# Optimization experiments

Measured on AMD Instinct MI355X. Metric: run time of the kernel, lower is better.

## Reference

```python
import jax, jax.numpy as jnp
import numpy as np

D_LOB = 128
D_HAWKES = 32
N_HEADS = 4
HEAD_DIM = D_LOB // N_HEADS
LN_EPS = 1e-5


def setup_inputs() -> dict:
    key = jax.random.key(0)
    ks = jax.random.split(key, 10)
    B, T = 8, 2048
    s = lambda fan_in: 1.0 / np.sqrt(fan_in)
    return {
        "lob": jax.random.normal(ks[0], (B, T, D_LOB), dtype=jnp.float32),
        "hawkes": jax.random.normal(ks[1], (B, T, D_HAWKES), dtype=jnp.float32),
        # hawkes_proj: Linear(d_hawkes, d_lob)
        "Wp": jax.random.uniform(ks[2], (D_LOB, D_HAWKES), jnp.float32, -s(D_HAWKES), s(D_HAWKES)),
        "bp": jnp.zeros((D_LOB,), jnp.float32),
        # MultiheadAttention packed in-projection (3*d_lob, d_lob) and out-projection
        "Win": jax.random.uniform(ks[3], (3 * D_LOB, D_LOB), jnp.float32, -s(D_LOB), s(D_LOB)),
        "bin_": jnp.zeros((3 * D_LOB,), jnp.float32),
        "Wo": jax.random.uniform(ks[4], (D_LOB, D_LOB), jnp.float32, -s(D_LOB), s(D_LOB)),
        "bo": jnp.zeros((D_LOB,), jnp.float32),
        # LayerNorm affine params
        "gamma": jnp.ones((D_LOB,), jnp.float32),
        "beta": jnp.zeros((D_LOB,), jnp.float32),
    }


def reference(lob, hawkes, Wp, bp, Win, bin_, Wo, bo, gamma, beta):
    B, T, _ = lob.shape
    # hawkes_proj
    h = hawkes @ Wp.T + bp  # (B, T, d_lob)
    # packed QKV projection (query=lob, key=value=h)
    q = lob @ Win[:D_LOB].T + bin_[:D_LOB]
    k = h @ Win[D_LOB:2 * D_LOB].T + bin_[D_LOB:2 * D_LOB]
    v = h @ Win[2 * D_LOB:].T + bin_[2 * D_LOB:]
    # split heads -> (B, H, T, hd)
    split = lambda x: x.reshape(B, T, N_HEADS, HEAD_DIM).transpose(0, 2, 1, 3)
    q, k, v = split(q), split(k), split(v)
    scale = 1.0 / np.sqrt(HEAD_DIM).astype(np.float32)
    scores = jnp.einsum("bhqd,bhkd->bhqk", q * scale, k)  # (B, H, T, T)
    attn = jax.nn.softmax(scores, axis=-1)
    # dropout(p=0.1) omitted: reference is eval/inference mode
    ctx = jnp.einsum("bhqk,bhkd->bhqd", attn, v)  # (B, H, T, hd)
    ctx = ctx.transpose(0, 2, 1, 3).reshape(B, T, D_LOB)
    fused = ctx @ Wo.T + bo
    # residual + LayerNorm
    x = lob + fused
    mu = jnp.mean(x, axis=-1, keepdims=True)
    var = jnp.mean(jnp.square(x - mu), axis=-1, keepdims=True)
    out = (x - mu) * jax.lax.rsqrt(var + LN_EPS) * gamma + beta
    attn_w = jnp.mean(attn, axis=1)  # average over heads (B, T, T)
    return out, attn_w
```

## Files before the change

kernel.cpp:

```cpp
#include <hip/hip_runtime.h>
#include <hip/hip_bf16.h>

#define TT 2048
#define BB 8
#define DD 128
#define HH 4
#define BT (BB*TT)
#define BH (BB*HH)
#define SCALE 0.1767766952966369f
#define S2LOG (SCALE * 1.4426950408889634f)

typedef __attribute__((ext_vector_type(8))) short short8;
typedef __attribute__((ext_vector_type(4))) short short4v;
typedef __attribute__((ext_vector_type(4))) float f32x4;
typedef __hip_bfloat16 bf16;

#define MFMA16(a,b,c) __builtin_amdgcn_mfma_f32_16x16x32_bf16(a,b,c,0,0,0)

static __device__ inline short8 ldg8(const bf16* p) {
  return *reinterpret_cast<const short8*>(p);
}
static __device__ inline short4v ldg4(const bf16* p) {
  return *reinterpret_cast<const short4v*>(p);
}
static __device__ inline float b2f(bf16 x) { return __bfloat162float(x); }
static __device__ inline short f2bs(float x) {
  bf16 h = __float2bfloat16(x);
  return *reinterpret_cast<short*>(&h);
}
static __device__ inline short8 ldcvt8(const float* p) {
  f32x4 f0 = *reinterpret_cast<const f32x4*>(p);
  f32x4 f1 = *reinterpret_cast<const f32x4*>(p + 4);
  short8 r;
  #pragma unroll
  for (int i = 0; i < 4; ++i) { r[i] = f2bs(f0[i]); r[4+i] = f2bs(f1[i]); }
  return r;
}
static __device__ inline short8 pack_v(const bf16* vp) {
  short4v lo = ldg4(vp);
  short4v hi = ldg4(vp + 16);
  short8 r;
  #pragma unroll
  for (int j = 0; j < 4; ++j) { r[j] = lo[j]; r[4+j] = hi[j]; }
  return r;
}

__global__ __launch_bounds__(256) void proj_kernel(
    const float* __restrict__ lob, const float* __restrict__ hawkes,
    const float* __restrict__ Wp, const float* __restrict__ bp,
    const float* __restrict__ Win, const float* __restrict__ binp,
    bf16* __restrict__ qg, bf16* __restrict__ kg, bf16* __restrict__ vtg) {
  __shared__ bf16 hT[32*136];
  __shared__ bf16 vT[128*40];
  int tid = threadIdx.x;
  int wave = tid >> 6, lane = tid & 63;
  int lr = lane & 15, lq = lane >> 4;
  int r0 = blockIdx.x * 32;
  int b  = r0 >> 11, t0 = r0 & 2047;
  f32x4 z = {0.f,0.f,0.f,0.f};

  short8 alob[2][4], ahk[2];
  #pragma unroll
  for (int mt = 0; mt < 2; ++mt) {
    const float* lp = lob + (size_t)(r0 + mt*16 + lr)*128;
    #pragma unroll
    for (int kt = 0; kt < 4; ++kt) alob[mt][kt] = ldcvt8(lp + kt*32 + lq*8);
    ahk[mt] = ldcvt8(hawkes + (size_t)(r0 + mt*16 + lr)*32 + lq*8);
  }

  for (int nt = wave; nt < 8; nt += 4) {
    int cn = nt*16;
    short8 bfrag = ldcvt8(Wp + (size_t)(cn + lr)*32 + lq*8);
    float bias = bp[cn + lr];
    #pragma unroll
    for (int mt = 0; mt < 2; ++mt) {
      f32x4 c = MFMA16(ahk[mt], bfrag, z);
      #pragma unroll
      for (int r = 0; r < 4; ++r)
        hT[(mt*16 + lq*4 + r)*136 + cn + lr] = __float2bfloat16(c[r] + bias);
    }
  }
  __syncthreads();

  short8 ah[2][4];
  #pragma unroll
  for (int mt = 0; mt < 2; ++mt)
    #pragma unroll
    for (int kt = 0; kt < 4; ++kt)
      ah[mt][kt] = *reinterpret_cast<const short8*>(&hT[(mt*16 + lr)*136 + kt*32 + lq*8]);

  for (int nt = wave; nt < 24; nt += 4) {
    int which = nt >> 3;
    int c = (nt & 7)*16 + lr;
    const float* wrow = Win + (size_t)(which*128 + c)*128;
    float bias = binp[which*128 + c];
    f32x4 acc0 = z, acc1 = z;
    #pragma unroll
    for (int kt = 0; kt < 4; ++kt) {
      short8 bfrag = ldcvt8(wrow + kt*32 + lq*8);
      if (which == 0) {
        acc0 = MFMA16(alob[0][kt], bfrag, acc0);
        acc1 = MFMA16(alob[1][kt], bfrag, acc1);
      } else {
        acc0 = MFMA16(ah[0][kt], bfrag, acc0);
        acc1 = MFMA16(ah[1][kt], bfrag, acc1);
      }
    }
    int head = c >> 5, dd = c & 31;
    #pragma unroll
    for (int mt = 0; mt < 2; ++mt) {
      f32x4 acc = mt ? acc1 : acc0;
      #pragma unroll
      for (int r = 0; r < 4; ++r) {
        int row = mt*16 + lq*4 + r;
        float val = acc[r] + bias;
        if (which == 0)
          qg[((size_t)(b*HH + head)*TT + t0 + row)*32 + dd] = __float2bfloat16(val);
        else if (which == 1)
          kg[((size_t)(b*HH + head)*TT + t0 + row)*32 + dd] = __float2bfloat16(val);
        else
          vT[c*40 + row] = __float2bfloat16(val);
      }
    }
  }
  __syncthreads();

  {
    int dd = tid >> 1, half = tid & 1;
    int bh = b*HH + (dd >> 5);
    short8 s0 = *reinterpret_cast<const short8*>(&vT[dd*40 + half*16]);
    short8 s1 = *reinterpret_cast<const short8*>(&vT[dd*40 + half*16 + 8]);
    bf16* dst = vtg + ((size_t)bh*32 + (dd & 31))*TT + t0 + half*16;
    *reinterpret_cast<short8*>(dst) = s0;
    *reinterpret_cast<short8*>(dst + 8) = s1;
  }
}

__global__ __launch_bounds__(256) void attn_kernel(const bf16* __restrict__ qg,
    const bf16* __restrict__ kg, const bf16* __restrict__ vtg,
    float* __restrict__ attn_out, float* __restrict__ ctxg) {
  int wg = (blockIdx.x & 7)*64 + (blockIdx.x >> 3);
  int b = wg >> 6, qt = wg & 63;
  int head = threadIdx.x >> 6, lane = threadIdx.x & 63;
  int lr = lane & 15, lq = lane >> 4;
  int bh = b*HH + head;
  __shared__ float plds[2][4][32*68];
  const bf16* qp = qg + ((size_t)(bh*TT) + qt*32)*32;
  const bf16* kb = kg + (size_t)(bh*TT)*32;
  const bf16* vb = vtg + (size_t)(bh*32)*TT;
  short8 a0 = ldg8(qp + lr*32 + lq*8);
  short8 a1 = ldg8(qp + (16+lr)*32 + lq*8);
  f32x4 z = {0.f,0.f,0.f,0.f};

  float rs0 = 0.f, rs1 = 0.f;
  for (int kt = 0; kt < 64; ++kt) {
    const bf16* kp = kb + (size_t)(kt*32)*32;
    short8 bk0 = ldg8(kp + lr*32 + lq*8);
    short8 bk1 = ldg8(kp + (16+lr)*32 + lq*8);
    f32x4 s0a = MFMA16(bk0, a0, z);
    f32x4 s0b = MFMA16(bk0, a1, z);
    f32x4 s1a = MFMA16(bk1, a0, z);
    f32x4 s1b = MFMA16(bk1, a1, z);
    #pragma unroll
    for (int r = 0; r < 4; ++r) {
      rs0 += exp2f(s0a[r]*S2LOG) + exp2f(s1a[r]*S2LOG);
      rs1 += exp2f(s0b[r]*S2LOG) + exp2f(s1b[r]*S2LOG);
    }
  }
  rs0 += __shfl_xor(rs0, 16, 64); rs0 += __shfl_xor(rs0, 32, 64);
  rs1 += __shfl_xor(rs1, 16, 64); rs1 += __shfl_xor(rs1, 32, 64);
  float lb0 = -log2f(rs0);
  float lb1 = -log2f(rs1);

  f32x4 acc00 = z, acc01 = z, acc10 = z, acc11 = z;
  short8 kf[2][4];
  short8 vf[2][4];
  #pragma unroll
  for (int s = 0; s < 4; ++s)
    kf[0][s] = ldg8(kb + (size_t)(s*16 + lr)*32 + lq*8);
  #pragma unroll
  for (int t32 = 0; t32 < 2; ++t32)
    #pragma unroll
    for (int dt = 0; dt < 2; ++dt)
      vf[0][t32*2+dt] = pack_v(vb + (size_t)(dt*16 + lr)*TT + t32*32 + lq*4);

  int rr = (int)threadIdx.x >> 3, c0 = ((int)threadIdx.x & 7)*8;
  float* awdst = attn_out + ((size_t)(b*TT + qt*32 + rr))*TT + c0;

  for (int kt0 = 0; kt0 < 32; kt0 += 2) {
    #pragma unroll
    for (int par = 0; par < 2; ++par) {
      int kt2 = kt0 + par;
      int kbase = kt2*64;
      if (kt2 < 31) {
        int nb = kbase + 64;
        #pragma unroll
        for (int s = 0; s < 4; ++s)
          kf[par^1][s] = ldg8(kb + (size_t)(nb + s*16 + lr)*32 + lq*8);
        #pragma unroll
        for (int t32 = 0; t32 < 2; ++t32)
          #pragma unroll
          for (int dt = 0; dt < 2; ++dt)
            vf[par^1][t32*2+dt] = pack_v(vb + (size_t)(dt*16 + lr)*TT + nb + t32*32 + lq*4);
      }
      short8 ap[2][2];
      #pragma unroll
      for (int qtile = 0; qtile < 2; ++qtile) {
        float lb = qtile ? lb1 : lb0;
        const short8& aq = qtile ? a1 : a0;
        #pragma unroll
        for (int s = 0; s < 4; ++s) {
          f32x4 sv = MFMA16(kf[par][s], aq, z);
          f32x4 p4;
          #pragma unroll
          for (int r = 0; r < 4; ++r) p4[r] = exp2f(fmaf(sv[r], S2LOG, lb));
          *reinterpret_cast<f32x4*>(
              &plds[par][head][(qtile*16 + lr)*68 + s*16 + lq*4]) = p4;
          #pragma unroll
          for (int r = 0; r < 4; ++r)
            ap[qtile][s>>1][(s&1)*4 + r] = f2bs(p4[r]);
        }
      }
      __syncthreads();
      {
        const float* p0 = &plds[par][0][rr*68 + c0];
        f32x4 u0 = *reinterpret_cast<const f32x4*>(p0);
        f32x4 u1 = *reinterpret_cast<const f32x4*>(p0 + 4);
        #pragma unroll
        for (int h = 1; h < 4; ++h) {
          const float* ph = &plds[par][h][rr*68 + c0];
          u0 += *reinterpret_cast<const f32x4*>(ph);
          u1 += *reinterpret_cast<const f32x4*>(ph + 4);
        }
        float* dst = awdst + kbase;
        *reinterpret_cast<f32x4*>(dst)     = u0 * 0.25f;
        *reinterpret_cast<f32x4*>(dst + 4) = u1 * 0.25f;
      }
      #pragma unroll
      for (int t32 = 0; t32 < 2; ++t32) {
        acc00 = MFMA16(ap[0][t32], vf[par][t32*2+0], acc00);
        acc01 = MFMA16(ap[0][t32], vf[par][t32*2+1], acc01);
        acc10 = MFMA16(ap[1][t32], vf[par][t32*2+0], acc10);
        acc11 = MFMA16(ap[1][t32], vf[par][t32*2+1], acc11);
      }
    }
  }
  #pragma unroll
  for (int r = 0; r < 4; ++r) {
    int row0 = lq*4 + r, row1 = row0 + 16;
    size_t base0 = ((size_t)(b*TT + qt*32 + row0))*128 + head*32;
    size_t base1 = ((size_t)(b*TT + qt*32 + row1))*128 + head*32;
    ctxg[base0 + lr]      = acc00[r];
    ctxg[base0 + 16 + lr] = acc01[r];
    ctxg[base1 + lr]      = acc10[r];
    ctxg[base1 + 16 + lr] = acc11[r];
  }
}

__global__ __launch_bounds__(256) void outln_kernel(const float* __restrict__ ctxg,
    const float* __restrict__ lob, const float* __restrict__ Wo,
    const float* __restrict__ bo, const float* __restrict__ gamma,
    const float* __restrict__ beta, float* __restrict__ outg) {
  __shared__ float sWo[128*132];
  __shared__ float sP[384];
  __shared__ float sCtx[4][128];
  __shared__ float sLob[4][128];
  int tid = threadIdx.x;
  for (int i = tid; i < 128*32; i += 256) {
    int c = i >> 5, d4 = (i & 31)*4;
    *reinterpret_cast<f32x4*>(&sWo[c*132 + d4]) =
        *reinterpret_cast<const f32x4*>(&Wo[(size_t)c*128 + d4]);
  }
  if (tid < 128) {
    sP[tid] = bo[tid]; sP[128+tid] = gamma[tid]; sP[256+tid] = beta[tid];
  }
  __syncthreads();
  int wave = tid >> 6, lane = tid & 63;
  for (int it = 0; it < 8; ++it) {
    int row = blockIdx.x*32 + it*4 + wave;
    const float* cg = ctxg + (size_t)row*128;
    const float* lg = lob + (size_t)row*128;
    sCtx[wave][lane]    = cg[lane];
    sCtx[wave][64+lane] = cg[64+lane];
    sLob[wave][lane]    = lg[lane];
    sLob[wave][64+lane] = lg[64+lane];
    float x0 = sP[lane] + sLob[wave][lane];
    float x1 = sP[64+lane] + sLob[wave][64+lane];
    const float* w0 = &sWo[lane*132];
    const float* w1 = &sWo[(64+lane)*132];
    const float* cx = sCtx[wave];
    #pragma unroll 8
    for (int d4 = 0; d4 < 32; ++d4) {
      f32x4 cv  = *reinterpret_cast<const f32x4*>(cx + d4*4);
      f32x4 wv0 = *reinterpret_cast<const f32x4*>(w0 + d4*4);
      f32x4 wv1 = *reinterpret_cast<const f32x4*>(w1 + d4*4);
      x0 += cv[0]*wv0[0] + cv[1]*wv0[1] + cv[2]*wv0[2] + cv[3]*wv0[3];
      x1 += cv[0]*wv1[0] + cv[1]*wv1[1] + cv[2]*wv1[2] + cv[3]*wv1[3];
    }
    float sum = x0 + x1;
    #pragma unroll
    for (int m = 1; m < 64; m <<= 1) sum += __shfl_xor(sum, m, 64);
    float mu = sum * (1.0f/128.0f);
    float d0 = x0 - mu, d1 = x1 - mu;
    float vs = d0*d0 + d1*d1;
    #pragma unroll
    for (int m = 1; m < 64; m <<= 1) vs += __shfl_xor(vs, m, 64);
    float rstd = rsqrtf(vs*(1.0f/128.0f) + 1e-5f);
    outg[(size_t)row*128 + lane]      = d0*rstd*sP[128+lane] + sP[256+lane];
    outg[(size_t)row*128 + 64 + lane] = d1*rstd*sP[192+lane] + sP[320+lane];
  }
}

extern "C" void kernel_launch(void* const* d_in, const int* in_sizes, int n_in,
                              void* d_out, int out_size, void* d_ws, size_t ws_size,
                              hipStream_t stream) {
  const float* lob    = (const float*)d_in[0];
  const float* hawkes = (const float*)d_in[1];
  const float* Wp     = (const float*)d_in[2];
  const float* bp     = (const float*)d_in[3];
  const float* Win    = (const float*)d_in[4];
  const float* binp   = (const float*)d_in[5];
  const float* Wo     = (const float*)d_in[6];
  const float* bo     = (const float*)d_in[7];
  const float* gamma  = (const float*)d_in[8];
  const float* beta   = (const float*)d_in[9];
  float* outg = (float*)d_out;
  float* attn_out = outg + (size_t)BT*128;

  char* ws = (char*)d_ws;
  bf16*  qg   = (bf16*)(ws);
  bf16*  kg   = (bf16*)(ws + (size_t)4*1024*1024);
  bf16*  vtg  = (bf16*)(ws + (size_t)8*1024*1024);
  float* ctxg = (float*)(ws + (size_t)12*1024*1024);

  proj_kernel<<<BT/32, 256, 0, stream>>>(lob, hawkes, Wp, bp, Win, binp, qg, kg, vtg);
  attn_kernel<<<BB*(TT/32), 256, 0, stream>>>(qg, kg, vtg, attn_out, ctxg);
  outln_kernel<<<512, 256, 0, stream>>>(ctxg, lob, Wo, bo, gamma, beta, outg);
}
```

Baseline: 322.8 us.

## Split attention keys across waves, average heads in registers, MFMA out-projection

The attention kernel now has each wave handle all four heads over a disjoint strided subset of key tiles. This lets the head-averaged attention weights be summed in registers and written straight to global memory, removing the per-tile LDS exchange and __syncthreads. Row sums and partial context accumulators are reduced across waves through shared memory, and the context is stored as bf16. The output-projection kernel switches to bf16 MFMA with a shared-memory LayerNorm and a single-pass variance, at the cost of extra rounding error and higher register pressure from 32 accumulators per wave.

```diff
diff --git a/kernel.cpp b/kernel.cpp
--- a/kernel.cpp
+++ b/kernel.cpp
@@ -1,5 +1,6 @@
 #include <hip/hip_runtime.h>
 #include <hip/hip_bf16.h>
+#include <math.h>
 
 #define TT 2048
 #define BB 8
@@ -23,7 +24,6 @@
 static __device__ inline short4v ldg4(const bf16* p) {
   return *reinterpret_cast<const short4v*>(p);
 }
-static __device__ inline float b2f(bf16 x) { return __bfloat162float(x); }
 static __device__ inline short f2bs(float x) {
   bf16 h = __float2bfloat16(x);
   return *reinterpret_cast<short*>(&h);
@@ -34,14 +34,6 @@
   short8 r;
   #pragma unroll
   for (int i = 0; i < 4; ++i) { r[i] = f2bs(f0[i]); r[4+i] = f2bs(f1[i]); }
-  return r;
-}
-static __device__ inline short8 pack_v(const bf16* vp) {
-  short4v lo = ldg4(vp);
-  short4v hi = ldg4(vp + 16);
-  short8 r;
-  #pragma unroll
-  for (int j = 0; j < 4; ++j) { r[j] = lo[j]; r[4+j] = hi[j]; }
   return r;
 }
 
@@ -138,176 +130,213 @@
 
 __global__ __launch_bounds__(256) void attn_kernel(const bf16* __restrict__ qg,
     const bf16* __restrict__ kg, const bf16* __restrict__ vtg,
-    float* __restrict__ attn_out, float* __restrict__ ctxg) {
-  int wg = (blockIdx.x & 7)*64 + (blockIdx.x >> 3);
-  int b = wg >> 6, qt = wg & 63;
-  int head = threadIdx.x >> 6, lane = threadIdx.x & 63;
+    float* __restrict__ attn_out, bf16* __restrict__ ctxg) {
+  int wgid = (blockIdx.x & 7)*64 + (blockIdx.x >> 3);
+  int b = wgid >> 6, qt = wgid & 63;
+  int wave = threadIdx.x >> 6, lane = threadIdx.x & 63;
   int lr = lane & 15, lq = lane >> 4;
-  int bh = b*HH + head;
-  __shared__ float plds[2][4][32*68];
-  const bf16* qp = qg + ((size_t)(bh*TT) + qt*32)*32;
-  const bf16* kb = kg + (size_t)(bh*TT)*32;
-  const bf16* vb = vtg + (size_t)(bh*32)*TT;
-  short8 a0 = ldg8(qp + lr*32 + lq*8);
-  short8 a1 = ldg8(qp + (16+lr)*32 + lq*8);
+  __shared__ float sRed[4][16*132];
+  float* sdl = &sRed[0][0];
+  const bf16* qb = qg + ((size_t)(b*HH)*TT + (size_t)qt*32)*32;
+  const bf16* kb = kg + (size_t)(b*HH)*TT*32;
+  const bf16* vb = vtg + (size_t)(b*HH)*32*TT;
   f32x4 z = {0.f,0.f,0.f,0.f};
 
-  float rs0 = 0.f, rs1 = 0.f;
-  for (int kt = 0; kt < 64; ++kt) {
-    const bf16* kp = kb + (size_t)(kt*32)*32;
-    short8 bk0 = ldg8(kp + lr*32 + lq*8);
-    short8 bk1 = ldg8(kp + (16+lr)*32 + lq*8);
-    f32x4 s0a = MFMA16(bk0, a0, z);
-    f32x4 s0b = MFMA16(bk0, a1, z);
-    f32x4 s1a = MFMA16(bk1, a0, z);
-    f32x4 s1b = MFMA16(bk1, a1, z);
-    #pragma unroll
-    for (int r = 0; r < 4; ++r) {
-      rs0 += exp2f(s0a[r]*S2LOG) + exp2f(s1a[r]*S2LOG);
-      rs1 += exp2f(s0b[r]*S2LOG) + exp2f(s1b[r]*S2LOG);
-    }
-  }
-  rs0 += __shfl_xor(rs0, 16, 64); rs0 += __shfl_xor(rs0, 32, 64);
-  rs1 += __shfl_xor(rs1, 16, 64); rs1 += __shfl_xor(rs1, 32, 64);
-  float lb0 = -log2f(rs0);
-  float lb1 = -log2f(rs1);
-
-  f32x4 acc00 = z, acc01 = z, acc10 = z, acc11 = z;
-  short8 kf[2][4];
-  short8 vf[2][4];
-  #pragma unroll
-  for (int s = 0; s < 4; ++s)
-    kf[0][s] = ldg8(kb + (size_t)(s*16 + lr)*32 + lq*8);
-  #pragma unroll
-  for (int t32 = 0; t32 < 2; ++t32)
-    #pragma unroll
-    for (int dt = 0; dt < 2; ++dt)
-      vf[0][t32*2+dt] = pack_v(vb + (size_t)(dt*16 + lr)*TT + t32*32 + lq*4);
-
-  int rr = (int)threadIdx.x >> 3, c0 = ((int)threadIdx.x & 7)*8;
-  float* awdst = attn_out + ((size_t)(b*TT + qt*32 + rr))*TT + c0;
-
-  for (int kt0 = 0; kt0 < 32; kt0 += 2) {
-    #pragma unroll
-    for (int par = 0; par < 2; ++par) {
-      int kt2 = kt0 + par;
-      int kbase = kt2*64;
-      if (kt2 < 31) {
-        int nb = kbase + 64;
-        #pragma unroll
-        for (int s = 0; s < 4; ++s)
-          kf[par^1][s] = ldg8(kb + (size_t)(nb + s*16 + lr)*32 + lq*8);
-        #pragma unroll
-        for (int t32 = 0; t32 < 2; ++t32)
-          #pragma unroll
-          for (int dt = 0; dt < 2; ++dt)
-            vf[par^1][t32*2+dt] = pack_v(vb + (size_t)(dt*16 + lr)*TT + nb + t32*32 + lq*4);
-      }
-      short8 ap[2][2];
-      #pragma unroll
-      for (int qtile = 0; qtile < 2; ++qtile) {
-        float lb = qtile ? lb1 : lb0;
-        const short8& aq = qtile ? a1 : a0;
-        #pragma unroll
-        for (int s = 0; s < 4; ++s) {
-          f32x4 sv = MFMA16(kf[par][s], aq, z);
-          f32x4 p4;
-          #pragma unroll
-          for (int r = 0; r < 4; ++r) p4[r] = exp2f(fmaf(sv[r], S2LOG, lb));
-          *reinterpret_cast<f32x4*>(
-              &plds[par][head][(qtile*16 + lr)*68 + s*16 + lq*4]) = p4;
-          #pragma unroll
-          for (int r = 0; r < 4; ++r)
-            ap[qtile][s>>1][(s&1)*4 + r] = f2bs(p4[r]);
+  short8 aq[4][2];
+  #pragma unroll
+  for (int h = 0; h < 4; ++h)
+    #pragma unroll
+    for (int m = 0; m < 2; ++m)
+      aq[h][m] = ldg8(qb + (size_t)h*TT*32 + (m*16 + lr)*32 + lq*8);
+
+  float rs[4][2] = {{0.f,0.f},{0.f,0.f},{0.f,0.f},{0.f,0.f}};
+  for (int i = 0; i < 32; ++i) {
+    int s = wave + i*4;
+    #pragma unroll
+    for (int h = 0; h < 4; ++h) {
+      short8 kf = ldg8(kb + (size_t)h*TT*32 + (s*16 + lr)*32 + lq*8);
+      #pragma unroll
+      for (int m = 0; m < 2; ++m) {
+        f32x4 sv = MFMA16(kf, aq[h][m], z);
+        #pragma unroll
+        for (int r = 0; r < 4; ++r) rs[h][m] += exp2f(sv[r]*S2LOG);
+      }
+    }
+  }
+  #pragma unroll
+  for (int h = 0; h < 4; ++h)
+    #pragma unroll
+    for (int m = 0; m < 2; ++m) {
+      rs[h][m] += __shfl_xor(rs[h][m], 16, 64);
+      rs[h][m] += __shfl_xor(rs[h][m], 32, 64);
+    }
+  if (lq == 0) {
+    #pragma unroll
+    for (int h = 0; h < 4; ++h)
+      #pragma unroll
+      for (int m = 0; m < 2; ++m)
+        sdl[wave*128 + h*32 + m*16 + lr] = rs[h][m];
+  }
+  __syncthreads();
+  float lb[4][2];
+  #pragma unroll
+  for (int h = 0; h < 4; ++h)
+    #pragma unroll
+    for (int m = 0; m < 2; ++m) {
+      float t = sdl[0*128 + h*32 + m*16 + lr] + sdl[1*128 + h*32 + m*16 + lr]
+              + sdl[2*128 + h*32 + m*16 + lr] + sdl[3*128 + h*32 + m*16 + lr];
+      lb[h][m] = -log2f(t);
+    }
+  __syncthreads();
+
+  f32x4 acc[4][2][2];
+  #pragma unroll
+  for (int h = 0; h < 4; ++h)
+    #pragma unroll
+    for (int m = 0; m < 2; ++m)
+      #pragma unroll
+      for (int dt = 0; dt < 2; ++dt) acc[h][m][dt] = z;
+
+  float* awr = attn_out + (size_t)(b*TT + qt*32)*TT;
+  for (int i = 0; i < 16; ++i) {
+    int sA = wave + i*8, sB = sA + 4;
+    f32x4 awA0 = z, awA1 = z, awB0 = z, awB1 = z;
+    #pragma unroll
+    for (int h = 0; h < 4; ++h) {
+      const bf16* kph = kb + (size_t)h*TT*32;
+      short8 kfA = ldg8(kph + (sA*16 + lr)*32 + lq*8);
+      short8 kfB = ldg8(kph + (sB*16 + lr)*32 + lq*8);
+      short8 apm[2];
+      #pragma unroll
+      for (int m = 0; m < 2; ++m) {
+        f32x4 svA = MFMA16(kfA, aq[h][m], z);
+        f32x4 svB = MFMA16(kfB, aq[h][m], z);
+        f32x4 pA, pB;
+        #pragma unroll
+        for (int r = 0; r < 4; ++r) {
+          pA[r] = exp2f(fmaf(svA[r], S2LOG, lb[h][m]));
+          pB[r] = exp2f(fmaf(svB[r], S2LOG, lb[h][m]));
         }
-      }
-      __syncthreads();
-      {
-        const float* p0 = &plds[par][0][rr*68 + c0];
-        f32x4 u0 = *reinterpret_cast<const f32x4*>(p0);
-        f32x4 u1 = *reinterpret_cast<const f32x4*>(p0 + 4);
-        #pragma unroll
-        for (int h = 1; h < 4; ++h) {
-          const float* ph = &plds[par][h][rr*68 + c0];
-          u0 += *reinterpret_cast<const f32x4*>(ph);
-          u1 += *reinterpret_cast<const f32x4*>(ph + 4);
-        }
-        float* dst = awdst + kbase;
-        *reinterpret_cast<f32x4*>(dst)     = u0 * 0.25f;
-        *reinterpret_cast<f32x4*>(dst + 4) = u1 * 0.25f;
-      }
-      #pragma unroll
-      for (int t32 = 0; t32 < 2; ++t32) {
-        acc00 = MFMA16(ap[0][t32], vf[par][t32*2+0], acc00);
-        acc01 = MFMA16(ap[0][t32], vf[par][t32*2+1], acc01);
-        acc10 = MFMA16(ap[1][t32], vf[par][t32*2+0], acc10);
-        acc11 = MFMA16(ap[1][t32], vf[par][t32*2+1], acc11);
-      }
-    }
-  }
-  #pragma unroll
-  for (int r = 0; r < 4; ++r) {
-    int row0 = lq*4 + r, row1 = row0 + 16;
-    size_t base0 = ((size_t)(b*TT + qt*32 + row0))*128 + head*32;
-    size_t base1 = ((size_t)(b*TT + qt*32 + row1))*128 + head*32;
-    ctxg[base0 + lr]      = acc00[r];
-    ctxg[base0 + 16 + lr] = acc01[r];
-    ctxg[base1 + lr]      = acc10[r];
-    ctxg[base1 + 16 + lr] = acc11[r];
-  }
-}
-
-__global__ __launch_bounds__(256) void outln_kernel(const float* __restrict__ ctxg,
+        if (m == 0) { awA0 += pA; awB0 += pB; } else { awA1 += pA; awB1 += pB; }
+        short8 ap;
+        #pragma unroll
+        for (int r = 0; r < 4; ++r) { ap[r] = f2bs(pA[r]); ap[4+r] = f2bs(pB[r]); }
+        apm[m] = ap;
+      }
+      const bf16* vph = vb + (size_t)h*32*TT;
+      #pragma unroll
+      for (int dt = 0; dt < 2; ++dt) {
+        const bf16* vp = vph + (size_t)(dt*16 + lr)*TT;
+        short4v lo = ldg4(vp + sA*16 + lq*4);
+        short4v hi = ldg4(vp + sB*16 + lq*4);
+        short8 vf;
+        #pragma unroll
+        for (int j = 0; j < 4; ++j) { vf[j] = lo[j]; vf[4+j] = hi[j]; }
+        acc[h][0][dt] = MFMA16(apm[0], vf, acc[h][0][dt]);
+        acc[h][1][dt] = MFMA16(apm[1], vf, acc[h][1][dt]);
+      }
+    }
+    *reinterpret_cast<f32x4*>(awr + (size_t)lr*TT      + sA*16 + lq*4) = awA0 * 0.25f;
+    *reinterpret_cast<f32x4*>(awr + (size_t)lr*TT      + sB*16 + lq*4) = awB0 * 0.25f;
+    *reinterpret_cast<f32x4*>(awr + (size_t)(16+lr)*TT + sA*16 + lq*4) = awA1 * 0.25f;
+    *reinterpret_cast<f32x4*>(awr + (size_t)(16+lr)*TT + sB*16 + lq*4) = awB1 * 0.25f;
+  }
+
+  bf16* cbase = ctxg + (size_t)(b*TT + qt*32)*128;
+  #pragma unroll
+  for (int m = 0; m < 2; ++m) {
+    #pragma unroll
+    for (int h = 0; h < 4; ++h)
+      #pragma unroll
+      for (int dt = 0; dt < 2; ++dt)
+        #pragma unroll
+        for (int r = 0; r < 4; ++r)
+          sRed[wave][(lq*4 + r)*132 + h*32 + dt*16 + lr] = acc[h][m][dt][r];
+    __syncthreads();
+    {
+      int t = threadIdx.x;
+      int q = t >> 4, d0 = (t & 15)*8;
+      float v[8];
+      #pragma unroll
+      for (int j = 0; j < 8; ++j)
+        v[j] = sRed[0][q*132 + d0 + j] + sRed[1][q*132 + d0 + j]
+             + sRed[2][q*132 + d0 + j] + sRed[3][q*132 + d0 + j];
+      short8 o;
+      #pragma unroll
+      for (int j = 0; j < 8; ++j) o[j] = f2bs(v[j]);
+      *reinterpret_cast<short8*>(cbase + (size_t)(m*16 + q)*128 + d0) = o;
+    }
+    __syncthreads();
+  }
+}
+
+__global__ __launch_bounds__(256) void outln_kernel(const bf16* __restrict__ ctxg,
     const float* __restrict__ lob, const float* __restrict__ Wo,
     const float* __restrict__ bo, const float* __restrict__ gamma,
     const float* __restrict__ beta, float* __restrict__ outg) {
-  __shared__ float sWo[128*132];
-  __shared__ float sP[384];
-  __shared__ float sCtx[4][128];
-  __shared__ float sLob[4][128];
-  int tid = threadIdx.x;
-  for (int i = tid; i < 128*32; i += 256) {
-    int c = i >> 5, d4 = (i & 31)*4;
-    *reinterpret_cast<f32x4*>(&sWo[c*132 + d4]) =
-        *reinterpret_cast<const f32x4*>(&Wo[(size_t)c*128 + d4]);
-  }
-  if (tid < 128) {
-    sP[tid] = bo[tid]; sP[128+tid] = gamma[tid]; sP[256+tid] = beta[tid];
-  }
-  __syncthreads();
-  int wave = tid >> 6, lane = tid & 63;
-  for (int it = 0; it < 8; ++it) {
-    int row = blockIdx.x*32 + it*4 + wave;
-    const float* cg = ctxg + (size_t)row*128;
-    const float* lg = lob + (size_t)row*128;
-    sCtx[wave][lane]    = cg[lane];
-    sCtx[wave][64+lane] = cg[64+lane];
-    sLob[wave][lane]    = lg[lane];
-    sLob[wave][64+lane] = lg[64+lane];
-    float x0 = sP[lane] + sLob[wave][lane];
-    float x1 = sP[64+lane] + sLob[wave][64+lane];
-    const float* w0 = &sWo[lane*132];
-    const float* w1 = &sWo[(64+lane)*132];
-    const float* cx = sCtx[wave];
-    #pragma unroll 8
-    for (int d4 = 0; d4 < 32; ++d4) {
-      f32x4 cv  = *reinterpret_cast<const f32x4*>(cx + d4*4);
-      f32x4 wv0 = *reinterpret_cast<const f32x4*>(w0 + d4*4);
-      f32x4 wv1 = *reinterpret_cast<const f32x4*>(w1 + d4*4);
-      x0 += cv[0]*wv0[0] + cv[1]*wv0[1] + cv[2]*wv0[2] + cv[3]*wv0[3];
-      x1 += cv[0]*wv1[0] + cv[1]*wv1[1] + cv[2]*wv1[2] + cv[3]*wv1[3];
-    }
-    float sum = x0 + x1;
-    #pragma unroll
-    for (int m = 1; m < 64; m <<= 1) sum += __shfl_xor(sum, m, 64);
+  __shared__ float sX[32*132];
+  __shared__ float sPar[256];
+  int tid = threadIdx.x, wave = tid >> 6, lane = tid & 63;
+  int lr = lane & 15, lq = lane >> 4;
+  int r0 = blockIdx.x * 32;
+  if (tid < 128) { sPar[tid] = gamma[tid]; sPar[128+tid] = beta[tid]; }
+  f32x4 z = {0.f,0.f,0.f,0.f};
+  short8 actx[2][4];
+  #pragma unroll
+  for (int mt = 0; mt < 2; ++mt)
+    #pragma unroll
+    for (int kt = 0; kt < 4; ++kt)
+      actx[mt][kt] = ldg8(ctxg + (size_t)(r0 + mt*16 + lr)*128 + kt*32 + lq*8);
+  for (int nt = wave; nt < 8; nt += 4) {
+    f32x4 acc0 = z, acc1 = z;
+    #pragma unroll
+    for (int kt = 0; kt < 4; ++kt) {
+      short8 bfrag = ldcvt8(Wo + (size_t)(nt*16 + lr)*128 + kt*32 + lq*8);
+      acc0 = MFMA16(actx[0][kt], bfrag, acc0);
+      acc1 = MFMA16(actx[1][kt], bfrag, acc1);
+    }
+    int d = nt*16 + lr;
+    float bias = bo[d];
+    #pragma unroll
+    for (int mt = 0; mt < 2; ++mt) {
+      f32x4 acc = mt ? acc1 : acc0;
+      #pragma unroll
+      for (int r = 0; r < 4; ++r) {
+        int row = mt*16 + lq*4 + r;
+        sX[row*132 + d] = acc[r] + bias + lob[(size_t)(r0 + row)*128 + d];
+      }
+    }
+  }
+  __syncthreads();
+  {
+    int row = tid >> 3, j = tid & 7;
+    const float* xp = &sX[row*132 + j*16];
+    f32x4 x[4];
+    #pragma unroll
+    for (int v = 0; v < 4; ++v) x[v] = *reinterpret_cast<const f32x4*>(xp + v*4);
+    float sum = 0.f, sq = 0.f;
+    #pragma unroll
+    for (int v = 0; v < 4; ++v)
+      #pragma unroll
+      for (int e = 0; e < 4; ++e) { sum += x[v][e]; sq += x[v][e]*x[v][e]; }
+    #pragma unroll
+    for (int mdx = 1; mdx < 8; mdx <<= 1) {
+      sum += __shfl_xor(sum, mdx, 64);
+      sq  += __shfl_xor(sq,  mdx, 64);
+    }
     float mu = sum * (1.0f/128.0f);
-    float d0 = x0 - mu, d1 = x1 - mu;
-    float vs = d0*d0 + d1*d1;
-    #pragma unroll
-    for (int m = 1; m < 64; m <<= 1) vs += __shfl_xor(vs, m, 64);
-    float rstd = rsqrtf(vs*(1.0f/128.0f) + 1e-5f);
-    outg[(size_t)row*128 + lane]      = d0*rstd*sP[128+lane] + sP[256+lane];
-    outg[(size_t)row*128 + 64 + lane] = d1*rstd*sP[192+lane] + sP[320+lane];
+    float rstd = rsqrtf(sq*(1.0f/128.0f) - mu*mu + 1e-5f);
+    float* op = outg + (size_t)(r0 + row)*128 + j*16;
+    #pragma unroll
+    for (int v = 0; v < 4; ++v) {
+      f32x4 o;
+      #pragma unroll
+      for (int e = 0; e < 4; ++e) {
+        int d = j*16 + v*4 + e;
+        o[e] = (x[v][e] - mu)*rstd*sPar[d] + sPar[128+d];
+      }
+      *reinterpret_cast<f32x4*>(op + v*4) = o;
+    }
   }
 }
 
@@ -331,7 +360,7 @@
   bf16*  qg   = (bf16*)(ws);
   bf16*  kg   = (bf16*)(ws + (size_t)4*1024*1024);
   bf16*  vtg  = (bf16*)(ws + (size_t)8*1024*1024);
-  float* ctxg = (float*)(ws + (size_t)12*1024*1024);
+  bf16*  ctxg = (bf16*)(ws + (size_t)12*1024*1024);
 
   proj_kernel<<<BT/32, 256, 0, stream>>>(lob, hawkes, Wp, bp, Win, binp, qg, kg, vtg);
   attn_kernel<<<BB*(TT/32), 256, 0, stream>>>(qg, kg, vtg, attn_out, ctxg);
```

Measured after the change: 328.6 us. Within noise of the previous version (+1.8%).
